# Kernel tuning notes

Hardware: AMD Instinct MI355X
Metric: run time of the kernel (lower is better)

## Reference

```python
import jax, jax.numpy as jnp
import numpy as np

H = 32  # hidden size (hard-coded in the torch module)

def _lstm_layer(x, W_ih, W_hh):
    # x: [B, T, F]; W_ih: [4H, F]; W_hh: [4H, H]; bias=False
    B = x.shape[0]
    # precompute input projection for all timesteps: [T, B, 4H]
    xg = jnp.einsum('btf,gf->tbg', x, W_ih)
    WhhT = W_hh.T  # [H, 4H]
    def step(carry, xg_t):
        h, c = carry
        gates = xg_t + h @ WhhT          # [B, 4H]
        i, f, g, o = jnp.split(gates, 4, axis=-1)  # PyTorch gate order i,f,g,o
        i = jax.nn.sigmoid(i)
        f = jax.nn.sigmoid(f)
        g = jnp.tanh(g)
        o = jax.nn.sigmoid(o)
        c = f * c + i * g
        h = o * jnp.tanh(c)
        return (h, c), h
    h0 = jnp.zeros((B, H), x.dtype)
    c0 = jnp.zeros((B, H), x.dtype)
    (hT, cT), hs = jax.lax.scan(step, (h0, c0), xg)
    return jnp.transpose(hs, (1, 0, 2)), hT, cT  # outputs [B,T,H], final h, final c


def setup_inputs() -> dict:
    key = jax.random.key(0)
    ks = jax.random.split(key, 8)
    B, T, F = 8192, 60, 158
    s_in = 1.0 / np.sqrt(H)  # PyTorch LSTM init scale
    inp = {
        'x':     jax.random.normal(ks[0], (B, T, F), jnp.float32),
        'W_ih0': jax.random.uniform(ks[1], (4 * H, F), jnp.float32, -s_in, s_in),
        'W_hh0': jax.random.uniform(ks[2], (4 * H, H), jnp.float32, -s_in, s_in),
        'W_ih1': jax.random.uniform(ks[3], (4 * H, H), jnp.float32, -s_in, s_in),
        'W_hh1': jax.random.uniform(ks[4], (4 * H, H), jnp.float32, -s_in, s_in),
        'W1':    jax.random.uniform(ks[5], (16, H), jnp.float32, -s_in, s_in),
        'b1':    jax.random.uniform(ks[6], (16,), jnp.float32, -s_in, s_in),
        'W2':    jax.random.uniform(ks[7], (1, 16), jnp.float32, -0.25, 0.25),
    }
    return inp


def reference(x, W_ih0, W_hh0, W_ih1, W_hh1, W1, b1, W2):
    out1, h1, c1 = _lstm_layer(x, W_ih0, W_hh0)      # layer 1 (inter-layer dropout inactive at eval)
    out2, h2, c2 = _lstm_layer(out1, W_ih1, W_hh1)   # layer 2
    # torch code: output, h_n = lstm(x) -> h_n is the TUPLE (h_n, c_n),
    # so h_n[-1] == c_n with shape [num_layers=2, B, H]
    c_n = jnp.stack([c1, c2], axis=0)                 # [2, B, H]
    y = jax.nn.relu(c_n @ W1.T + b1) @ W2.T           # [2, B, 1]
    return y
```

## Files before the change

### kernel.cpp

```cpp
#include <hip/hip_runtime.h>


constexpr int Bn = 8192, Tn = 60, Fn = 158, Hn = 32;
constexpr int SKX = 168;
constexpr int SKH = 40;
constexpr int SG = 132;
constexpr float LS = 4096.f;
constexpr float ILS = 1.f / 4096.f;

typedef _Float16 half8 __attribute__((ext_vector_type(8)));
typedef __fp16 half2f __attribute__((ext_vector_type(2)));
typedef __attribute__((ext_vector_type(4))) float floatx4;

__device__ __forceinline__ float sigm_(float x) {
    return __fdividef(1.f, 1.f + __expf(-x));
}
__device__ __forceinline__ float tanh_(float x) {
    return 1.f - __fdividef(2.f, __expf(2.f * x) + 1.f);
}
__device__ __forceinline__ unsigned h2u(half2f h) {
    return __builtin_bit_cast(unsigned, h);
}
__device__ __forceinline__ void cvt8h(const float* v, half8& hi, half8& lo) {
#pragma unroll
    for (int j = 0; j < 8; j += 2) {
        half2f h = __builtin_amdgcn_cvt_pkrtz(v[j], v[j + 1]);
        float r0 = (v[j] - (float)h[0]) * LS;
        float r1 = (v[j + 1] - (float)h[1]) * LS;
        half2f l = __builtin_amdgcn_cvt_pkrtz(r0, r1);
        hi[j] = (_Float16)h[0]; hi[j + 1] = (_Float16)h[1];
        lo[j] = (_Float16)l[0]; lo[j + 1] = (_Float16)l[1];
    }
}

__global__ __launch_bounds__(256, 2) void lstm2_fused_kernel(
    const float* __restrict__ x,
    const float* __restrict__ Wih0, const float* __restrict__ Whh0,
    const float* __restrict__ Wih1, const float* __restrict__ Whh1,
    const float* __restrict__ W1, const float* __restrict__ b1,
    const float* __restrict__ W2, float* __restrict__ out) {
    __shared__ unsigned short sXh[2 * 16 * SKX];
    __shared__ unsigned short sXl[2 * 16 * SKX];
    __shared__ unsigned short sH1h[16 * SKH], sH1l[16 * SKH];
    __shared__ unsigned short sH2h[16 * SKH], sH2l[16 * SKH];
    __shared__ float sG1[16 * SG];
    __shared__ float sG2[16 * SG];

    const int tid = threadIdx.x;
    const int wave = tid >> 6, lane = tid & 63;
    const int quad = lane >> 4, l15 = lane & 15;
    const int bBase = blockIdx.x * 16;

    half8 bX[5][2][2];
#pragma unroll
    for (int nt = 0; nt < 2; ++nt) {
        const int n = wave * 32 + nt * 16 + l15;
#pragma unroll
        for (int ks = 0; ks < 5; ++ks) {
            float wv[8];
#pragma unroll
            for (int j = 0; j < 8; ++j) {
                int k = ks * 32 + quad * 8 + j;
                wv[j] = (k < Fn) ? Wih0[n * Fn + k] : 0.f;
            }
            cvt8h(wv, bX[ks][nt][0], bX[ks][nt][1]);
        }
    }
    half8 bW[3][2][2];
    const float* Wp[3] = {Whh0, Wih1, Whh1};
#pragma unroll
    for (int m = 0; m < 3; ++m)
#pragma unroll
        for (int nt = 0; nt < 2; ++nt) {
            const int n = wave * 32 + nt * 16 + l15;
            const float* wp = Wp[m] + n * Hn + quad * 8;
            float4 q0 = *(const float4*)(wp);
            float4 q1 = *(const float4*)(wp + 4);
            float wv[8] = {q0.x, q0.y, q0.z, q0.w, q1.x, q1.y, q1.z, q1.w};
            cvt8h(wv, bW[m][nt][0], bW[m][nt][1]);
        }

    const float* xp[5];
    int soff[5];
    bool act[5];
#pragma unroll
    for (int r = 0; r < 5; ++r) {
        int i = tid + r * 256;
        act[r] = (i < 1264);
        int row = i / 79, c = i - row * 79;
        if (!act[r]) { row = 0; c = 0; }
        soff[r] = row * (SKX / 2) + c;
        xp[r] = x + (size_t)(bBase + row) * (Tn * Fn) + 2 * c;
    }
    auto stage = [&](const float2* v, int buf) {
        unsigned* dh = (unsigned*)sXh + buf * (16 * SKX / 2);
        unsigned* dl = (unsigned*)sXl + buf * (16 * SKX / 2);
#pragma unroll
        for (int r = 0; r < 5; ++r) {
            if (act[r]) {
                half2f h = __builtin_amdgcn_cvt_pkrtz(v[r].x, v[r].y);
                half2f l = __builtin_amdgcn_cvt_pkrtz(
                    (v[r].x - (float)h[0]) * LS, (v[r].y - (float)h[1]) * LS);
                dh[soff[r]] = h2u(h);
                dl[soff[r]] = h2u(l);
            }
        }
    };

    for (int i = tid; i < 320; i += 256) {
        ((unsigned*)sH1h)[i] = 0; ((unsigned*)sH1l)[i] = 0;
        ((unsigned*)sH2h)[i] = 0; ((unsigned*)sH2l)[i] = 0;
    }
    if (tid < 32) {
        int buf = tid >> 4, row = tid & 15;
        ((unsigned*)sXh)[buf * 1344 + row * 84 + 79] = 0;
        ((unsigned*)sXl)[buf * 1344 + row * 84 + 79] = 0;
    }

#pragma unroll
    for (int t0 = 0; t0 < 2; ++t0) {
        float2 v[5];
#pragma unroll
        for (int r = 0; r < 5; ++r) {
            v[r] = act[r] ? *(const float2*)xp[r] : make_float2(0.f, 0.f);
            xp[r] += Fn;
        }
        stage(v, t0);
    }

    const int aOffH = l15 * SKH + quad * 8;
    const int urow = tid >> 4, hp = (tid & 15) * 2;
    float c1x = 0.f, c1y = 0.f, c2x = 0.f, c2y = 0.f;

    auto upd = [&](const float* sGx, unsigned short* sHh, unsigned short* sHl,
                   float& cx, float& cy) {
        const float* g = sGx + urow * SG + hp * 4;
        float4 A = *(const float4*)g;
        float4 Bv = *(const float4*)(g + 4);
        cx = sigm_(A.y) * cx + sigm_(A.x) * tanh_(A.z);
        cy = sigm_(Bv.y) * cy + sigm_(Bv.x) * tanh_(Bv.z);
        float h0 = sigm_(A.w) * tanh_(cx);
        float h1v = sigm_(Bv.w) * tanh_(cy);
        half2f hh = __builtin_amdgcn_cvt_pkrtz(h0, h1v);
        half2f hl = __builtin_amdgcn_cvt_pkrtz((h0 - (float)hh[0]) * LS,
                                               (h1v - (float)hh[1]) * LS);
        *(unsigned*)(sHh + urow * SKH + hp) = h2u(hh);
        *(unsigned*)(sHl + urow * SKH + hp) = h2u(hl);
    };

    __syncthreads();

    {
        floatx4 aH[2] = {}, aL[2] = {};
#pragma unroll
        for (int ks = 0; ks < 5; ++ks) {
            const int off = l15 * SKX + ks * 32 + quad * 8;
            half8 xh = *(const half8*)(sXh + off);
            half8 xl = *(const half8*)(sXl + off);
#pragma unroll
            for (int nt = 0; nt < 2; ++nt) {
                aH[nt] = __builtin_amdgcn_mfma_f32_16x16x32_f16(xh, bX[ks][nt][0], aH[nt], 0, 0, 0);
                aL[nt] = __builtin_amdgcn_mfma_f32_16x16x32_f16(xh, bX[ks][nt][1], aL[nt], 0, 0, 0);
                aL[nt] = __builtin_amdgcn_mfma_f32_16x16x32_f16(xl, bX[ks][nt][0], aL[nt], 0, 0, 0);
            }
        }
#pragma unroll
        for (int nt = 0; nt < 2; ++nt)
#pragma unroll
            for (int reg = 0; reg < 4; ++reg)
                sG1[(quad * 4 + reg) * SG + (nt * 16 + l15) * 4 + wave] =
                    fmaf(ILS, aL[nt][reg], aH[nt][reg]);
    }
    __syncthreads();
    upd(sG1, sH1h, sH1l, c1x, c1y);
    __syncthreads();

    for (int i = 0; i < Tn - 1; ++i) {
        float2 xr[5];
        const bool pf = (i + 2 < Tn);
        if (pf) {
#pragma unroll
            for (int r = 0; r < 5; ++r) {
                xr[r] = act[r] ? *(const float2*)xp[r] : make_float2(0.f, 0.f);
                xp[r] += Fn;
            }
        }
        {
            const unsigned short* bxh = sXh + ((i + 1) & 1) * (16 * SKX);
            const unsigned short* bxl = sXl + ((i + 1) & 1) * (16 * SKX);
            half8 a1h = *(const half8*)(sH1h + aOffH);
            half8 a1l = *(const half8*)(sH1l + aOffH);
            half8 a2h = *(const half8*)(sH2h + aOffH);
            half8 a2l = *(const half8*)(sH2l + aOffH);
            floatx4 a1H[2] = {}, a1L[2] = {}, a2H[2] = {}, a2L[2] = {};
#pragma unroll
            for (int ks = 0; ks < 5; ++ks) {
                const int off = l15 * SKX + ks * 32 + quad * 8;
                half8 xh = *(const half8*)(bxh + off);
                half8 xl = *(const half8*)(bxl + off);
#pragma unroll
                for (int nt = 0; nt < 2; ++nt) {
                    a1H[nt] = __builtin_amdgcn_mfma_f32_16x16x32_f16(xh, bX[ks][nt][0], a1H[nt], 0, 0, 0);
                    a1L[nt] = __builtin_amdgcn_mfma_f32_16x16x32_f16(xh, bX[ks][nt][1], a1L[nt], 0, 0, 0);
                    a1L[nt] = __builtin_amdgcn_mfma_f32_16x16x32_f16(xl, bX[ks][nt][0], a1L[nt], 0, 0, 0);
                }
            }
#pragma unroll
            for (int nt = 0; nt < 2; ++nt) {
                a1H[nt] = __builtin_amdgcn_mfma_f32_16x16x32_f16(a1h, bW[0][nt][0], a1H[nt], 0, 0, 0);
                a1L[nt] = __builtin_amdgcn_mfma_f32_16x16x32_f16(a1h, bW[0][nt][1], a1L[nt], 0, 0, 0);
                a1L[nt] = __builtin_amdgcn_mfma_f32_16x16x32_f16(a1l, bW[0][nt][0], a1L[nt], 0, 0, 0);
                a2H[nt] = __builtin_amdgcn_mfma_f32_16x16x32_f16(a1h, bW[1][nt][0], a2H[nt], 0, 0, 0);
                a2L[nt] = __builtin_amdgcn_mfma_f32_16x16x32_f16(a1h, bW[1][nt][1], a2L[nt], 0, 0, 0);
                a2L[nt] = __builtin_amdgcn_mfma_f32_16x16x32_f16(a1l, bW[1][nt][0], a2L[nt], 0, 0, 0);
                a2H[nt] = __builtin_amdgcn_mfma_f32_16x16x32_f16(a2h, bW[2][nt][0], a2H[nt], 0, 0, 0);
                a2L[nt] = __builtin_amdgcn_mfma_f32_16x16x32_f16(a2h, bW[2][nt][1], a2L[nt], 0, 0, 0);
                a2L[nt] = __builtin_amdgcn_mfma_f32_16x16x32_f16(a2l, bW[2][nt][0], a2L[nt], 0, 0, 0);
            }
#pragma unroll
            for (int nt = 0; nt < 2; ++nt)
#pragma unroll
                for (int reg = 0; reg < 4; ++reg) {
                    const int idx = (quad * 4 + reg) * SG + (nt * 16 + l15) * 4 + wave;
                    sG1[idx] = fmaf(ILS, a1L[nt][reg], a1H[nt][reg]);
                    sG2[idx] = fmaf(ILS, a2L[nt][reg], a2H[nt][reg]);
                }
        }
        if (pf) stage(xr, i & 1);
        __syncthreads();
        upd(sG2, sH2h, sH2l, c2x, c2y);
        upd(sG1, sH1h, sH1l, c1x, c1y);
        __syncthreads();
    }

    {
        half8 a1h = *(const half8*)(sH1h + aOffH);
        half8 a1l = *(const half8*)(sH1l + aOffH);
        half8 a2h = *(const half8*)(sH2h + aOffH);
        half8 a2l = *(const half8*)(sH2l + aOffH);
        floatx4 aH[2] = {}, aL[2] = {};
#pragma unroll
        for (int nt = 0; nt < 2; ++nt) {
            aH[nt] = __builtin_amdgcn_mfma_f32_16x16x32_f16(a1h, bW[1][nt][0], aH[nt], 0, 0, 0);
            aL[nt] = __builtin_amdgcn_mfma_f32_16x16x32_f16(a1h, bW[1][nt][1], aL[nt], 0, 0, 0);
            aL[nt] = __builtin_amdgcn_mfma_f32_16x16x32_f16(a1l, bW[1][nt][0], aL[nt], 0, 0, 0);
            aH[nt] = __builtin_amdgcn_mfma_f32_16x16x32_f16(a2h, bW[2][nt][0], aH[nt], 0, 0, 0);
            aL[nt] = __builtin_amdgcn_mfma_f32_16x16x32_f16(a2h, bW[2][nt][1], aL[nt], 0, 0, 0);
            aL[nt] = __builtin_amdgcn_mfma_f32_16x16x32_f16(a2l, bW[2][nt][0], aL[nt], 0, 0, 0);
        }
#pragma unroll
        for (int nt = 0; nt < 2; ++nt)
#pragma unroll
            for (int reg = 0; reg < 4; ++reg)
                sG2[(quad * 4 + reg) * SG + (nt * 16 + l15) * 4 + wave] =
                    fmaf(ILS, aL[nt][reg], aH[nt][reg]);
    }
    __syncthreads();
    {
        const float* g = sG2 + urow * SG + hp * 4;
        float4 A = *(const float4*)g;
        float4 Bv = *(const float4*)(g + 4);
        c2x = sigm_(A.y) * c2x + sigm_(A.x) * tanh_(A.z);
        c2y = sigm_(Bv.y) * c2y + sigm_(Bv.x) * tanh_(Bv.z);
    }

    float* sC = sG1;
    *(float2*)(sC + urow * 33 + hp) = make_float2(c1x, c1y);
    *(float2*)(sC + 528 + urow * 33 + hp) = make_float2(c2x, c2y);
    __syncthreads();
    if (tid < 32) {
        int l = tid >> 4, b = tid & 15;
        const float* cc = sC + l * 528 + b * 33;
        float y = 0.f;
#pragma unroll 1
        for (int q = 0; q < 16; ++q) {
            float s = b1[q];
#pragma unroll
            for (int j = 0; j < 32; ++j) s = fmaf(cc[j], W1[q * 32 + j], s);
            y = fmaf(fmaxf(s, 0.f), W2[q], y);
        }
        out[l * Bn + bBase + b] = y;
    }
}

extern "C" void kernel_launch(void* const* d_in, const int* in_sizes, int n_in,
                              void* d_out, int out_size, void* d_ws, size_t ws_size,
                              hipStream_t stream) {
    const float* x    = (const float*)d_in[0];
    const float* Wih0 = (const float*)d_in[1];
    const float* Whh0 = (const float*)d_in[2];
    const float* Wih1 = (const float*)d_in[3];
    const float* Whh1 = (const float*)d_in[4];
    const float* W1   = (const float*)d_in[5];
    const float* b1   = (const float*)d_in[6];
    const float* W2   = (const float*)d_in[7];
    float* out = (float*)d_out;

    lstm2_fused_kernel<<<Bn / 16, 256, 0, stream>>>(x, Wih0, Whh0, Wih1, Whh1,
                                                    W1, b1, W2, out);
}
```

Baseline: 473.6 us.

## Transpose MFMA so gate quadruples land in registers, drop gate LDS round-trip

Permutes the weight rows so that each lane's four MFMA accumulator registers hold the i,f,g,o gates of one hidden unit, swapping the A and B operands so the output is gates-by-batch. The LSTM cell update then runs directly on the accumulators, which removes the shared-memory gate buffers and one of the two barriers per timestep. The hidden state is double-buffered by parity so the next step's reads do not race with this step's writes. The cost is scattered 16-bit LDS stores of h, and the elementwise work is redistributed across lanes.

```diff
diff --git a/kernel.cpp b/kernel.cpp
--- a/kernel.cpp
+++ b/kernel.cpp
@@ -4,13 +4,12 @@
 constexpr int Bn = 8192, Tn = 60, Fn = 158, Hn = 32;
 constexpr int SKX = 168;
 constexpr int SKH = 40;
-constexpr int SG = 132;
 constexpr float LS = 4096.f;
 constexpr float ILS = 1.f / 4096.f;
 
 typedef _Float16 half8 __attribute__((ext_vector_type(8)));
 typedef __fp16 half2f __attribute__((ext_vector_type(2)));
-typedef __attribute__((ext_vector_type(4))) float floatx4;
+typedef float floatx4 __attribute__((ext_vector_type(4)));
 
 __device__ __forceinline__ float sigm_(float x) {
     return __fdividef(1.f, 1.f + __expf(-x));
@@ -41,29 +40,27 @@
     const float* __restrict__ W2, float* __restrict__ out) {
     __shared__ unsigned short sXh[2 * 16 * SKX];
     __shared__ unsigned short sXl[2 * 16 * SKX];
-    __shared__ unsigned short sH1h[16 * SKH], sH1l[16 * SKH];
-    __shared__ unsigned short sH2h[16 * SKH], sH2l[16 * SKH];
-    __shared__ float sG1[16 * SG];
-    __shared__ float sG2[16 * SG];
+    __shared__ unsigned short sH[2][2][2][16 * SKH];
 
     const int tid = threadIdx.x;
     const int wave = tid >> 6, lane = tid & 63;
     const int quad = lane >> 4, l15 = lane & 15;
     const int bBase = blockIdx.x * 16;
+    const int hl = l15 >> 2, gi = l15 & 3;
 
     half8 bX[5][2][2];
 #pragma unroll
-    for (int nt = 0; nt < 2; ++nt) {
-        const int n = wave * 32 + nt * 16 + l15;
+    for (int mt = 0; mt < 2; ++mt) {
+        const int grow = gi * 32 + wave * 8 + mt * 4 + hl;
 #pragma unroll
         for (int ks = 0; ks < 5; ++ks) {
             float wv[8];
 #pragma unroll
             for (int j = 0; j < 8; ++j) {
                 int k = ks * 32 + quad * 8 + j;
-                wv[j] = (k < Fn) ? Wih0[n * Fn + k] : 0.f;
-            }
-            cvt8h(wv, bX[ks][nt][0], bX[ks][nt][1]);
+                wv[j] = (k < Fn) ? Wih0[grow * Fn + k] : 0.f;
+            }
+            cvt8h(wv, bX[ks][mt][0], bX[ks][mt][1]);
         }
     }
     half8 bW[3][2][2];
@@ -71,13 +68,13 @@
 #pragma unroll
     for (int m = 0; m < 3; ++m)
 #pragma unroll
-        for (int nt = 0; nt < 2; ++nt) {
-            const int n = wave * 32 + nt * 16 + l15;
-            const float* wp = Wp[m] + n * Hn + quad * 8;
+        for (int mt = 0; mt < 2; ++mt) {
+            const int grow = gi * 32 + wave * 8 + mt * 4 + hl;
+            const float* wp = Wp[m] + grow * Hn + quad * 8;
             float4 q0 = *(const float4*)(wp);
             float4 q1 = *(const float4*)(wp + 4);
             float wv[8] = {q0.x, q0.y, q0.z, q0.w, q1.x, q1.y, q1.z, q1.w};
-            cvt8h(wv, bW[m][nt][0], bW[m][nt][1]);
+            cvt8h(wv, bW[m][mt][0], bW[m][mt][1]);
         }
 
     const float* xp[5];
@@ -107,10 +104,7 @@
         }
     };
 
-    for (int i = tid; i < 320; i += 256) {
-        ((unsigned*)sH1h)[i] = 0; ((unsigned*)sH1l)[i] = 0;
-        ((unsigned*)sH2h)[i] = 0; ((unsigned*)sH2l)[i] = 0;
-    }
+    for (int i = tid; i < 2560; i += 256) ((unsigned*)sH)[i] = 0;
     if (tid < 32) {
         int buf = tid >> 4, row = tid & 15;
         ((unsigned*)sXh)[buf * 1344 + row * 84 + 79] = 0;
@@ -128,24 +122,17 @@
         stage(v, t0);
     }
 
-    const int aOffH = l15 * SKH + quad * 8;
-    const int urow = tid >> 4, hp = (tid & 15) * 2;
-    float c1x = 0.f, c1y = 0.f, c2x = 0.f, c2y = 0.f;
-
-    auto upd = [&](const float* sGx, unsigned short* sHh, unsigned short* sHl,
-                   float& cx, float& cy) {
-        const float* g = sGx + urow * SG + hp * 4;
-        float4 A = *(const float4*)g;
-        float4 Bv = *(const float4*)(g + 4);
-        cx = sigm_(A.y) * cx + sigm_(A.x) * tanh_(A.z);
-        cy = sigm_(Bv.y) * cy + sigm_(Bv.x) * tanh_(Bv.z);
-        float h0 = sigm_(A.w) * tanh_(cx);
-        float h1v = sigm_(Bv.w) * tanh_(cy);
+    const int hOffR = l15 * SKH + quad * 8;
+    const int hW = l15 * SKH + wave * 8 + quad;
+    float c1[2] = {0.f, 0.f}, c2[2] = {0.f, 0.f};
+
+    auto packStore = [&](float h0, float h1v, unsigned short* dh, unsigned short* dl) {
         half2f hh = __builtin_amdgcn_cvt_pkrtz(h0, h1v);
-        half2f hl = __builtin_amdgcn_cvt_pkrtz((h0 - (float)hh[0]) * LS,
+        half2f ll = __builtin_amdgcn_cvt_pkrtz((h0 - (float)hh[0]) * LS,
                                                (h1v - (float)hh[1]) * LS);
-        *(unsigned*)(sHh + urow * SKH + hp) = h2u(hh);
-        *(unsigned*)(sHl + urow * SKH + hp) = h2u(hl);
+        unsigned uh = h2u(hh), ul = h2u(ll);
+        dh[hW] = (unsigned short)uh; dh[hW + 4] = (unsigned short)(uh >> 16);
+        dl[hW] = (unsigned short)ul; dl[hW + 4] = (unsigned short)(ul >> 16);
     };
 
     __syncthreads();
@@ -158,21 +145,24 @@
             half8 xh = *(const half8*)(sXh + off);
             half8 xl = *(const half8*)(sXl + off);
 #pragma unroll
-            for (int nt = 0; nt < 2; ++nt) {
-                aH[nt] = __builtin_amdgcn_mfma_f32_16x16x32_f16(xh, bX[ks][nt][0], aH[nt], 0, 0, 0);
-                aL[nt] = __builtin_amdgcn_mfma_f32_16x16x32_f16(xh, bX[ks][nt][1], aL[nt], 0, 0, 0);
-                aL[nt] = __builtin_amdgcn_mfma_f32_16x16x32_f16(xl, bX[ks][nt][0], aL[nt], 0, 0, 0);
-            }
-        }
-#pragma unroll
-        for (int nt = 0; nt < 2; ++nt)
-#pragma unroll
-            for (int reg = 0; reg < 4; ++reg)
-                sG1[(quad * 4 + reg) * SG + (nt * 16 + l15) * 4 + wave] =
-                    fmaf(ILS, aL[nt][reg], aH[nt][reg]);
-    }
-    __syncthreads();
-    upd(sG1, sH1h, sH1l, c1x, c1y);
+            for (int mt = 0; mt < 2; ++mt) {
+                aH[mt] = __builtin_amdgcn_mfma_f32_16x16x32_f16(bX[ks][mt][0], xh, aH[mt], 0, 0, 0);
+                aL[mt] = __builtin_amdgcn_mfma_f32_16x16x32_f16(bX[ks][mt][1], xh, aL[mt], 0, 0, 0);
+                aL[mt] = __builtin_amdgcn_mfma_f32_16x16x32_f16(bX[ks][mt][0], xl, aL[mt], 0, 0, 0);
+            }
+        }
+        float hv[2];
+#pragma unroll
+        for (int mt = 0; mt < 2; ++mt) {
+            float gI = fmaf(ILS, aL[mt][0], aH[mt][0]);
+            float gF = fmaf(ILS, aL[mt][1], aH[mt][1]);
+            float gG = fmaf(ILS, aL[mt][2], aH[mt][2]);
+            float gO = fmaf(ILS, aL[mt][3], aH[mt][3]);
+            c1[mt] = sigm_(gF) * c1[mt] + sigm_(gI) * tanh_(gG);
+            hv[mt] = sigm_(gO) * tanh_(c1[mt]);
+        }
+        packStore(hv[0], hv[1], sH[0][0][0], sH[0][0][1]);
+    }
     __syncthreads();
 
     for (int i = 0; i < Tn - 1; ++i) {
@@ -185,88 +175,91 @@
                 xp[r] += Fn;
             }
         }
-        {
-            const unsigned short* bxh = sXh + ((i + 1) & 1) * (16 * SKX);
-            const unsigned short* bxl = sXl + ((i + 1) & 1) * (16 * SKX);
-            half8 a1h = *(const half8*)(sH1h + aOffH);
-            half8 a1l = *(const half8*)(sH1l + aOffH);
-            half8 a2h = *(const half8*)(sH2h + aOffH);
-            half8 a2l = *(const half8*)(sH2l + aOffH);
-            floatx4 a1H[2] = {}, a1L[2] = {}, a2H[2] = {}, a2L[2] = {};
-#pragma unroll
-            for (int ks = 0; ks < 5; ++ks) {
-                const int off = l15 * SKX + ks * 32 + quad * 8;
-                half8 xh = *(const half8*)(bxh + off);
-                half8 xl = *(const half8*)(bxl + off);
-#pragma unroll
-                for (int nt = 0; nt < 2; ++nt) {
-                    a1H[nt] = __builtin_amdgcn_mfma_f32_16x16x32_f16(xh, bX[ks][nt][0], a1H[nt], 0, 0, 0);
-                    a1L[nt] = __builtin_amdgcn_mfma_f32_16x16x32_f16(xh, bX[ks][nt][1], a1L[nt], 0, 0, 0);
-                    a1L[nt] = __builtin_amdgcn_mfma_f32_16x16x32_f16(xl, bX[ks][nt][0], a1L[nt], 0, 0, 0);
-                }
-            }
-#pragma unroll
-            for (int nt = 0; nt < 2; ++nt) {
-                a1H[nt] = __builtin_amdgcn_mfma_f32_16x16x32_f16(a1h, bW[0][nt][0], a1H[nt], 0, 0, 0);
-                a1L[nt] = __builtin_amdgcn_mfma_f32_16x16x32_f16(a1h, bW[0][nt][1], a1L[nt], 0, 0, 0);
-                a1L[nt] = __builtin_amdgcn_mfma_f32_16x16x32_f16(a1l, bW[0][nt][0], a1L[nt], 0, 0, 0);
-                a2H[nt] = __builtin_amdgcn_mfma_f32_16x16x32_f16(a1h, bW[1][nt][0], a2H[nt], 0, 0, 0);
-                a2L[nt] = __builtin_amdgcn_mfma_f32_16x16x32_f16(a1h, bW[1][nt][1], a2L[nt], 0, 0, 0);
-                a2L[nt] = __builtin_amdgcn_mfma_f32_16x16x32_f16(a1l, bW[1][nt][0], a2L[nt], 0, 0, 0);
-                a2H[nt] = __builtin_amdgcn_mfma_f32_16x16x32_f16(a2h, bW[2][nt][0], a2H[nt], 0, 0, 0);
-                a2L[nt] = __builtin_amdgcn_mfma_f32_16x16x32_f16(a2h, bW[2][nt][1], a2L[nt], 0, 0, 0);
-                a2L[nt] = __builtin_amdgcn_mfma_f32_16x16x32_f16(a2l, bW[2][nt][0], a2L[nt], 0, 0, 0);
-            }
-#pragma unroll
-            for (int nt = 0; nt < 2; ++nt)
-#pragma unroll
-                for (int reg = 0; reg < 4; ++reg) {
-                    const int idx = (quad * 4 + reg) * SG + (nt * 16 + l15) * 4 + wave;
-                    sG1[idx] = fmaf(ILS, a1L[nt][reg], a1H[nt][reg]);
-                    sG2[idx] = fmaf(ILS, a2L[nt][reg], a2H[nt][reg]);
-                }
-        }
+        const int par = i & 1;
+        const unsigned short* bxh = sXh + ((i + 1) & 1) * (16 * SKX);
+        const unsigned short* bxl = sXl + ((i + 1) & 1) * (16 * SKX);
+        half8 f1h = *(const half8*)(sH[par][0][0] + hOffR);
+        half8 f1l = *(const half8*)(sH[par][0][1] + hOffR);
+        half8 f2h = *(const half8*)(sH[par][1][0] + hOffR);
+        half8 f2l = *(const half8*)(sH[par][1][1] + hOffR);
+        floatx4 a1H[2] = {}, a1L[2] = {}, a2H[2] = {}, a2L[2] = {};
+#pragma unroll
+        for (int ks = 0; ks < 5; ++ks) {
+            const int off = l15 * SKX + ks * 32 + quad * 8;
+            half8 xh = *(const half8*)(bxh + off);
+            half8 xl = *(const half8*)(bxl + off);
+#pragma unroll
+            for (int mt = 0; mt < 2; ++mt) {
+                a1H[mt] = __builtin_amdgcn_mfma_f32_16x16x32_f16(bX[ks][mt][0], xh, a1H[mt], 0, 0, 0);
+                a1L[mt] = __builtin_amdgcn_mfma_f32_16x16x32_f16(bX[ks][mt][1], xh, a1L[mt], 0, 0, 0);
+                a1L[mt] = __builtin_amdgcn_mfma_f32_16x16x32_f16(bX[ks][mt][0], xl, a1L[mt], 0, 0, 0);
+            }
+        }
+#pragma unroll
+        for (int mt = 0; mt < 2; ++mt) {
+            a1H[mt] = __builtin_amdgcn_mfma_f32_16x16x32_f16(bW[0][mt][0], f1h, a1H[mt], 0, 0, 0);
+            a1L[mt] = __builtin_amdgcn_mfma_f32_16x16x32_f16(bW[0][mt][1], f1h, a1L[mt], 0, 0, 0);
+            a1L[mt] = __builtin_amdgcn_mfma_f32_16x16x32_f16(bW[0][mt][0], f1l, a1L[mt], 0, 0, 0);
+            a2H[mt] = __builtin_amdgcn_mfma_f32_16x16x32_f16(bW[1][mt][0], f1h, a2H[mt], 0, 0, 0);
+            a2L[mt] = __builtin_amdgcn_mfma_f32_16x16x32_f16(bW[1][mt][1], f1h, a2L[mt], 0, 0, 0);
+            a2L[mt] = __builtin_amdgcn_mfma_f32_16x16x32_f16(bW[1][mt][0], f1l, a2L[mt], 0, 0, 0);
+            a2H[mt] = __builtin_amdgcn_mfma_f32_16x16x32_f16(bW[2][mt][0], f2h, a2H[mt], 0, 0, 0);
+            a2L[mt] = __builtin_amdgcn_mfma_f32_16x16x32_f16(bW[2][mt][1], f2h, a2L[mt], 0, 0, 0);
+            a2L[mt] = __builtin_amdgcn_mfma_f32_16x16x32_f16(bW[2][mt][0], f2l, a2L[mt], 0, 0, 0);
+        }
+        float h1v[2], h2v[2];
+#pragma unroll
+        for (int mt = 0; mt < 2; ++mt) {
+            float gI = fmaf(ILS, a2L[mt][0], a2H[mt][0]);
+            float gF = fmaf(ILS, a2L[mt][1], a2H[mt][1]);
+            float gG = fmaf(ILS, a2L[mt][2], a2H[mt][2]);
+            float gO = fmaf(ILS, a2L[mt][3], a2H[mt][3]);
+            c2[mt] = sigm_(gF) * c2[mt] + sigm_(gI) * tanh_(gG);
+            h2v[mt] = sigm_(gO) * tanh_(c2[mt]);
+            gI = fmaf(ILS, a1L[mt][0], a1H[mt][0]);
+            gF = fmaf(ILS, a1L[mt][1], a1H[mt][1]);
+            gG = fmaf(ILS, a1L[mt][2], a1H[mt][2]);
+            gO = fmaf(ILS, a1L[mt][3], a1H[mt][3]);
+            c1[mt] = sigm_(gF) * c1[mt] + sigm_(gI) * tanh_(gG);
+            h1v[mt] = sigm_(gO) * tanh_(c1[mt]);
+        }
+        packStore(h1v[0], h1v[1], sH[par ^ 1][0][0], sH[par ^ 1][0][1]);
+        packStore(h2v[0], h2v[1], sH[par ^ 1][1][0], sH[par ^ 1][1][1]);
         if (pf) stage(xr, i & 1);
         __syncthreads();
-        upd(sG2, sH2h, sH2l, c2x, c2y);
-        upd(sG1, sH1h, sH1l, c1x, c1y);
-        __syncthreads();
     }
 
     {
-        half8 a1h = *(const half8*)(sH1h + aOffH);
-        half8 a1l = *(const half8*)(sH1l + aOffH);
-        half8 a2h = *(const half8*)(sH2h + aOffH);
-        half8 a2l = *(const half8*)(sH2l + aOffH);
+        const int par = (Tn - 1) & 1;
+        half8 f1h = *(const half8*)(sH[par][0][0] + hOffR);
+        half8 f1l = *(const half8*)(sH[par][0][1] + hOffR);
+        half8 f2h = *(const half8*)(sH[par][1][0] + hOffR);
+        half8 f2l = *(const half8*)(sH[par][1][1] + hOffR);
         floatx4 aH[2] = {}, aL[2] = {};
 #pragma unroll
-        for (int nt = 0; nt < 2; ++nt) {
-            aH[nt] = __builtin_amdgcn_mfma_f32_16x16x32_f16(a1h, bW[1][nt][0], aH[nt], 0, 0, 0);
-            aL[nt] = __builtin_amdgcn_mfma_f32_16x16x32_f16(a1h, bW[1][nt][1], aL[nt], 0, 0, 0);
-            aL[nt] = __builtin_amdgcn_mfma_f32_16x16x32_f16(a1l, bW[1][nt][0], aL[nt], 0, 0, 0);
-            aH[nt] = __builtin_amdgcn_mfma_f32_16x16x32_f16(a2h, bW[2][nt][0], aH[nt], 0, 0, 0);
-            aL[nt] = __builtin_amdgcn_mfma_f32_16x16x32_f16(a2h, bW[2][nt][1], aL[nt], 0, 0, 0);
-            aL[nt] = __builtin_amdgcn_mfma_f32_16x16x32_f16(a2l, bW[2][nt][0], aL[nt], 0, 0, 0);
-        }
-#pragma unroll
-        for (int nt = 0; nt < 2; ++nt)
-#pragma unroll
-            for (int reg = 0; reg < 4; ++reg)
-                sG2[(quad * 4 + reg) * SG + (nt * 16 + l15) * 4 + wave] =
-                    fmaf(ILS, aL[nt][reg], aH[nt][reg]);
-    }
-    __syncthreads();
-    {
-        const float* g = sG2 + urow * SG + hp * 4;
-        float4 A = *(const float4*)g;
-        float4 Bv = *(const float4*)(g + 4);
-        c2x = sigm_(A.y) * c2x + sigm_(A.x) * tanh_(A.z);
-        c2y = sigm_(Bv.y) * c2y + sigm_(Bv.x) * tanh_(Bv.z);
-    }
-
-    float* sC = sG1;
-    *(float2*)(sC + urow * 33 + hp) = make_float2(c1x, c1y);
-    *(float2*)(sC + 528 + urow * 33 + hp) = make_float2(c2x, c2y);
+        for (int mt = 0; mt < 2; ++mt) {
+            aH[mt] = __builtin_amdgcn_mfma_f32_16x16x32_f16(bW[1][mt][0], f1h, aH[mt], 0, 0, 0);
+            aL[mt] = __builtin_amdgcn_mfma_f32_16x16x32_f16(bW[1][mt][1], f1h, aL[mt], 0, 0, 0);
+            aL[mt] = __builtin_amdgcn_mfma_f32_16x16x32_f16(bW[1][mt][0], f1l, aL[mt], 0, 0, 0);
+            aH[mt] = __builtin_amdgcn_mfma_f32_16x16x32_f16(bW[2][mt][0], f2h, aH[mt], 0, 0, 0);
+            aL[mt] = __builtin_amdgcn_mfma_f32_16x16x32_f16(bW[2][mt][1], f2h, aL[mt], 0, 0, 0);
+            aL[mt] = __builtin_amdgcn_mfma_f32_16x16x32_f16(bW[2][mt][0], f2l, aL[mt], 0, 0, 0);
+        }
+#pragma unroll
+        for (int mt = 0; mt < 2; ++mt) {
+            float gI = fmaf(ILS, aL[mt][0], aH[mt][0]);
+            float gF = fmaf(ILS, aL[mt][1], aH[mt][1]);
+            float gG = fmaf(ILS, aL[mt][2], aH[mt][2]);
+            c2[mt] = sigm_(gF) * c2[mt] + sigm_(gI) * tanh_(gG);
+        }
+    }
+
+    float* sC = (float*)sXh;
+#pragma unroll
+    for (int mt = 0; mt < 2; ++mt) {
+        sC[l15 * 33 + wave * 8 + mt * 4 + quad] = c1[mt];
+        sC[528 + l15 * 33 + wave * 8 + mt * 4 + quad] = c2[mt];
+    }
     __syncthreads();
     if (tid < 32) {
         int l = tid >> 4, b = tid & 15;
```

Result: faster. 461.8 us (-2.5%).
